# Performance work log

Hardware: AMD Instinct MI355X
Metric: run time of the kernel (lower is better)

Reference implementation:

```python
import jax, jax.numpy as jnp
import numpy as np


def _edge_index(n):
    # all ordered pairs (i, j), i != j -- static since n is a Python int
    ii = np.repeat(np.arange(n), n)
    jj = np.tile(np.arange(n), n)
    m = ii != jj
    return jnp.asarray(ii[m]), jnp.asarray(jj[m])


def _mlp2(x, w1, b1, w2, b2):
    # two Linear layers with ReLU after each (PointNet-style MLP([a,b,c]))
    h = jax.nn.relu(x @ w1 + b1)
    return jax.nn.relu(h @ w2 + b2)


def _fcn(x, w1, b1, w2, b2, w3, b3):
    # FullyConnectedNet: relu(fc1) -> relu(fc2) -> fc3 (no final relu)
    h = jax.nn.relu(x @ w1 + b1)
    h = jax.nn.relu(h @ w2 + b2)
    return h @ w3 + b3


def setup_inputs() -> dict:
    key = jax.random.key(0)
    ks = jax.random.split(key, 32)
    n = 256
    E = n * (n - 1)
    d = 512

    def lin(k, fin, fout):
        k1, k2 = jax.random.split(k)
        s = 1.0 / np.sqrt(fin)
        w = jax.random.uniform(k1, (fin, fout), jnp.float32, -s, s)
        b = jax.random.uniform(k2, (fout,), jnp.float32, -s, s)
        return w, b

    inp = {
        "insnum": n,
        "pred_codes": jax.random.normal(ks[0], (E, d), jnp.float32),
        "bboxes": jax.random.normal(ks[1], (n, 2, 3), jnp.float32),
        "lwhV": jax.random.uniform(ks[2], (n, 3), jnp.float32),
        "centroid": jax.random.normal(ks[3], (n, 3), jnp.float32),
    }
    inp["s_w1"], inp["s_b1"] = lin(ks[4], 512, 512)
    inp["s_w2"], inp["s_b2"] = lin(ks[5], 512, 512)
    inp["p_w1"], inp["p_b1"] = lin(ks[6], 512 + 128, 512)
    inp["p_w2"], inp["p_b2"] = lin(ks[7], 512, 512)
    inp["c_w1"], inp["c_b1"] = lin(ks[8], 512, 512)
    inp["c_w2"], inp["c_b2"] = lin(ks[9], 512, 512)
    inp["l_w1"], inp["l_b1"] = lin(ks[10], 512 * 3, 512)
    inp["l_w2"], inp["l_b2"] = lin(ks[11], 512, 512)
    inp["pos_w1"], inp["pos_b1"] = lin(ks[12], 5, 64)
    inp["pos_w2"], inp["pos_b2"] = lin(ks[13], 64, 64)
    inp["pos_w3"], inp["pos_b3"] = lin(ks[14], 64, 128)
    return inp


def reference(insnum, pred_codes, bboxes, lwhV, centroid,
              s_w1, s_b1, s_w2, s_b2,
              p_w1, p_b1, p_w2, p_b2,
              c_w1, c_b1, c_w2, c_b2,
              l_w1, l_b1, l_w2, l_b2,
              pos_w1, pos_b1, pos_w2, pos_b2, pos_w3, pos_b3):
    src, dst = _edge_index(insnum)
    ci = centroid[src, :2]          # [E, 2]
    cj = centroid[dst, :2]          # [E, 2]
    diff = ci - cj                  # vectorized replacement of per-edge loop
    distance = jnp.linalg.norm(diff, axis=1, keepdims=True)   # [E, 1]
    direction = diff / distance                                # [E, 2]
    pos_features = jnp.concatenate([diff, distance, direction], axis=1)  # [E, 5]

    support_codes = _mlp2(pred_codes, s_w1, s_b1, s_w2, s_b2)
    pos_codes = _fcn(pos_features, pos_w1, pos_b1, pos_w2, pos_b2, pos_w3, pos_b3)
    proximity_features = jnp.concatenate([pred_codes, pos_codes], axis=1)  # [E, 640]
    proximity_codes = _mlp2(proximity_features, p_w1, p_b1, p_w2, p_b2)
    comp_codes = _mlp2(pred_codes, c_w1, c_b1, c_w2, c_b2)
    link_in = jnp.concatenate([support_codes, proximity_codes, comp_codes], axis=1)  # [E, 1536]
    link_codes = _mlp2(link_in, l_w1, l_b1, l_w2, l_b2)
    return (link_codes, support_codes, proximity_codes, comp_codes)
```

## Files before the change

### kernel.cpp

```cpp
#include <hip/hip_runtime.h>
#include <stdint.h>

typedef unsigned short ushort_t;
typedef __attribute__((ext_vector_type(8))) short short8;
typedef __attribute__((ext_vector_type(8))) unsigned short u16x8;
typedef __attribute__((ext_vector_type(4))) float f32x4;

#define GLOBAL_AS __attribute__((address_space(1)))
#define LDS_AS __attribute__((address_space(3)))

__device__ __forceinline__ ushort_t f2bf(float f) {
  union { float f; uint32_t u; } v; v.f = f;
  uint32_t u = v.u;
  u += 0x7FFFu + ((u >> 16) & 1u);
  return (ushort_t)(u >> 16);
}

__device__ __forceinline__ int swz(int row, int byteInRow) {
  return (row * 128 + byteInRow) ^ ((row & 7) << 4);
}

struct TransArgs {
  const float* src[8];
  ushort_t* dst[8];
  int K[8];
  int blk0[9];
};

__global__ __launch_bounds__(256) void transpose_weights(TransArgs ta) {
  __shared__ float tile[64 * 65];
  int b = blockIdx.x;
  int mi = 0;
#pragma unroll
  for (int i = 1; i < 8; ++i) if (b >= ta.blk0[i]) mi = i;
  const float* src = ta.src[mi];
  ushort_t* dst = ta.dst[mi];
  int K = ta.K[mi];
  int rel = b - ta.blk0[mi];
  int ktiles = K >> 6;
  int k0 = (rel % ktiles) << 6;
  int n0 = (rel / ktiles) << 6;
  int t = threadIdx.x;
#pragma unroll
  for (int i = 0; i < 16; ++i) {
    int idx = i * 256 + t;
    int r = idx >> 6, c = idx & 63;
    tile[r * 65 + c] = src[(size_t)(k0 + r) * 512 + (n0 + c)];
  }
  __syncthreads();
#pragma unroll
  for (int i = 0; i < 16; ++i) {
    int idx = i * 256 + t;
    int r = idx >> 6, c = idx & 63;
    dst[(size_t)(n0 + r) * K + (k0 + c)] = f2bf(tile[c * 65 + r]);
  }
}

__global__ __launch_bounds__(256) void prep_kernel(
    const float* __restrict__ pred, const float* __restrict__ centroid,
    const float* __restrict__ pw1, const float* __restrict__ pb1,
    const float* __restrict__ pw2, const float* __restrict__ pb2,
    const float* __restrict__ pw3, const float* __restrict__ pb3,
    ushort_t* __restrict__ X, ushort_t* __restrict__ pos, int nm1)
{
  __shared__ ushort_t h1s[128 * 64];
  __shared__ ushort_t h2s[128 * 64];
  __shared__ ushort_t w2t[64 * 64];
  __shared__ ushort_t w3t[128 * 64];
  __shared__ float w1s[5 * 64];
  __shared__ float b1s[64], b2s[64], b3s[128];
  int t = threadIdx.x;
  for (int idx = t; idx < 64 * 64; idx += 256) {
    int k = idx >> 6, n = idx & 63;
    *(ushort_t*)((char*)w2t + swz(n, k * 2)) = f2bf(pw2[idx]);
  }
  for (int idx = t; idx < 64 * 128; idx += 256) {
    int k = idx >> 7, n = idx & 127;
    *(ushort_t*)((char*)w3t + swz(n, k * 2)) = f2bf(pw3[idx]);
  }
  for (int i = t; i < 5 * 64; i += 256) w1s[i] = pw1[i];
  if (t < 64) { b1s[t] = pb1[t]; b2s[t] = pb2[t]; }
  if (t < 128) b3s[t] = pb3[t];
  __syncthreads();

  int wid = t >> 6, lane = t & 63;
  int ebase = blockIdx.x * 128 + wid * 32;
  for (int it = 0; it < 32; ++it) {
    int e = ebase + it;
    const float* pr = pred + (size_t)e * 512 + lane * 8;
    float4 pA = *(const float4*)pr;
    float4 pB = *(const float4*)(pr + 4);
    u16x8 o;
    o[0] = f2bf(pA.x); o[1] = f2bf(pA.y); o[2] = f2bf(pA.z); o[3] = f2bf(pA.w);
    o[4] = f2bf(pB.x); o[5] = f2bf(pB.y); o[6] = f2bf(pB.z); o[7] = f2bf(pB.w);
    *(u16x8*)(X + (size_t)e * 512 + lane * 8) = o;
    int i = e / nm1;
    int r = e - i * nm1;
    int j = r + (r >= i ? 1 : 0);
    float dx = centroid[i * 3 + 0] - centroid[j * 3 + 0];
    float dy = centroid[i * 3 + 1] - centroid[j * 3 + 1];
    float dist = sqrtf(dx * dx + dy * dy);
    float inv = 1.0f / dist;
    float h1 = w1s[0 * 64 + lane] * dx + w1s[1 * 64 + lane] * dy + w1s[2 * 64 + lane] * dist
             + w1s[3 * 64 + lane] * (dx * inv) + w1s[4 * 64 + lane] * (dy * inv) + b1s[lane];
    h1 = fmaxf(h1, 0.0f);
    int row = wid * 32 + it;
    *(ushort_t*)((char*)h1s + swz(row, lane * 2)) = f2bf(h1);
  }
  __syncthreads();

  int colg = lane & 15, rowg = (lane >> 4) << 2;
  int ko_lane = (lane >> 4) * 8;
  {
    f32x4 acc[2][4];
    f32x4 zero = {0.0f, 0.0f, 0.0f, 0.0f};
#pragma unroll
    for (int m_ = 0; m_ < 2; ++m_)
#pragma unroll
      for (int n_ = 0; n_ < 4; ++n_) acc[m_][n_] = zero;
#pragma unroll
    for (int kk = 0; kk < 2; ++kk) {
      int ko = kk * 32 + ko_lane;
      short8 a[2], b[4];
#pragma unroll
      for (int m_ = 0; m_ < 2; ++m_)
        a[m_] = *(const short8*)((const char*)h1s + swz(wid * 32 + m_ * 16 + colg, ko * 2));
#pragma unroll
      for (int n_ = 0; n_ < 4; ++n_)
        b[n_] = *(const short8*)((const char*)w2t + swz(n_ * 16 + colg, ko * 2));
#pragma unroll
      for (int m_ = 0; m_ < 2; ++m_)
#pragma unroll
        for (int n_ = 0; n_ < 4; ++n_)
          acc[m_][n_] = __builtin_amdgcn_mfma_f32_16x16x32_bf16(a[m_], b[n_], acc[m_][n_], 0, 0, 0);
    }
#pragma unroll
    for (int n_ = 0; n_ < 4; ++n_) {
      int col = n_ * 16 + colg;
      float bv = b2s[col];
#pragma unroll
      for (int m_ = 0; m_ < 2; ++m_) {
        int row = wid * 32 + m_ * 16 + rowg;
#pragma unroll
        for (int jj = 0; jj < 4; ++jj) {
          float v = fmaxf(acc[m_][n_][jj] + bv, 0.0f);
          *(ushort_t*)((char*)h2s + swz(row + jj, col * 2)) = f2bf(v);
        }
      }
    }
  }
  __syncthreads();
  {
    f32x4 acc[2][8];
    f32x4 zero = {0.0f, 0.0f, 0.0f, 0.0f};
#pragma unroll
    for (int m_ = 0; m_ < 2; ++m_)
#pragma unroll
      for (int n_ = 0; n_ < 8; ++n_) acc[m_][n_] = zero;
#pragma unroll
    for (int kk = 0; kk < 2; ++kk) {
      int ko = kk * 32 + ko_lane;
      short8 a[2], b[8];
#pragma unroll
      for (int m_ = 0; m_ < 2; ++m_)
        a[m_] = *(const short8*)((const char*)h2s + swz(wid * 32 + m_ * 16 + colg, ko * 2));
#pragma unroll
      for (int n_ = 0; n_ < 8; ++n_)
        b[n_] = *(const short8*)((const char*)w3t + swz(n_ * 16 + colg, ko * 2));
#pragma unroll
      for (int m_ = 0; m_ < 2; ++m_)
#pragma unroll
        for (int n_ = 0; n_ < 8; ++n_)
          acc[m_][n_] = __builtin_amdgcn_mfma_f32_16x16x32_bf16(a[m_], b[n_], acc[m_][n_], 0, 0, 0);
    }
#pragma unroll
    for (int n_ = 0; n_ < 8; ++n_) {
      int col = n_ * 16 + colg;
      float bv = b3s[col];
#pragma unroll
      for (int m_ = 0; m_ < 2; ++m_) {
        int row = wid * 32 + m_ * 16 + rowg;
#pragma unroll
        for (int jj = 0; jj < 4; ++jj) {
          int e = blockIdx.x * 128 + row + jj;
          pos[(size_t)e * 128 + col] = f2bf(acc[m_][n_][jj] + bv);
        }
      }
    }
  }
}

__global__ __launch_bounds__(256) void gemm_bias_relu(
    const void* __restrict__ A0, int lda0,
    const void* __restrict__ A1, int lda1,
    const void* __restrict__ A2, int lda2,
    int s0, int s1, int aF32,
    const ushort_t* __restrict__ Bt, const float* __restrict__ bias,
    void* __restrict__ Cout, int outF32, ushort_t* __restrict__ Cdual, int K)
{
  __shared__ ushort_t As[128 * 64];
  __shared__ ushort_t Bs[128 * 64];
  int bid = blockIdx.x;
  int cpx = gridDim.x >> 3;
  int swzb = (bid & 7) * cpx + (bid >> 3);
  int mt = swzb >> 2, nt = swzb & 3;
  int m0 = mt << 7, n0 = nt << 7;
  int t = threadIdx.x;
  int lane = t & 63, wid = t >> 6;
  int wm = wid >> 1, wn = wid & 1;
  f32x4 acc[4][4];
  f32x4 zero = {0.0f, 0.0f, 0.0f, 0.0f};
#pragma unroll
  for (int a_ = 0; a_ < 4; ++a_)
#pragma unroll
    for (int b_ = 0; b_ < 4; ++b_) acc[a_][b_] = zero;

  for (int kt = 0; kt < K; kt += 64) {
    const void* Ab; int ldaA; int kin;
    if (kt < s0)      { Ab = A0; ldaA = lda0; kin = kt; }
    else if (kt < s1) { Ab = A1; ldaA = lda1; kin = kt - s0; }
    else              { Ab = A2; ldaA = lda2; kin = kt - s1; }
    if (aF32) {
      const float* Af = (const float*)Ab;
      int rr = t >> 1, cc0 = (t & 1) << 5;
      const float* g = Af + (size_t)(m0 + rr) * ldaA + kin + cc0;
      ushort_t* ldst = As + rr * 64 + cc0;
#pragma unroll
      for (int i = 0; i < 4; ++i) {
        float4 v0 = *(const float4*)(g + i * 8);
        float4 v1 = *(const float4*)(g + i * 8 + 4);
        u16x8 o;
        o[0] = f2bf(v0.x); o[1] = f2bf(v0.y); o[2] = f2bf(v0.z); o[3] = f2bf(v0.w);
        o[4] = f2bf(v1.x); o[5] = f2bf(v1.y); o[6] = f2bf(v1.z); o[7] = f2bf(v1.w);
        *(u16x8*)(ldst + i * 8) = o;
      }
    } else {
      const ushort_t* Ah = (const ushort_t*)Ab;
#pragma unroll
      for (int i = 0; i < 4; ++i) {
        int ch = i * 256 + t;
        int rr = ch >> 3, cc = (ch & 7) << 3;
        const ushort_t* g = Ah + (size_t)(m0 + rr) * ldaA + kin + cc;
        __builtin_amdgcn_global_load_lds((const GLOBAL_AS void*)g,
                                         (LDS_AS void*)(As + ch * 8), 16, 0, 0);
      }
    }
#pragma unroll
    for (int i = 0; i < 4; ++i) {
      int ch = i * 256 + t;
      int rr = ch >> 3, cc = (ch & 7) << 3;
      const ushort_t* g = Bt + (size_t)(n0 + rr) * K + kt + cc;
      __builtin_amdgcn_global_load_lds((const GLOBAL_AS void*)g,
                                       (LDS_AS void*)(Bs + ch * 8), 16, 0, 0);
    }
    __syncthreads();
#pragma unroll
    for (int kk = 0; kk < 64; kk += 32) {
      int ko = kk + (lane >> 4) * 8;
      short8 a[4], b[4];
#pragma unroll
      for (int m_ = 0; m_ < 4; ++m_)
        a[m_] = *(const short8*)(As + (wm * 64 + m_ * 16 + (lane & 15)) * 64 + ko);
#pragma unroll
      for (int n_ = 0; n_ < 4; ++n_)
        b[n_] = *(const short8*)(Bs + (wn * 64 + n_ * 16 + (lane & 15)) * 64 + ko);
#pragma unroll
      for (int m_ = 0; m_ < 4; ++m_)
#pragma unroll
        for (int n_ = 0; n_ < 4; ++n_)
          acc[m_][n_] = __builtin_amdgcn_mfma_f32_16x16x32_bf16(a[m_], b[n_], acc[m_][n_], 0, 0, 0);
    }
    __syncthreads();
  }
  int colg = lane & 15, rowg = (lane >> 4) << 2;
  float* C32 = (float*)Cout;
  ushort_t* C16 = (ushort_t*)Cout;
#pragma unroll
  for (int n_ = 0; n_ < 4; ++n_) {
    int col = n0 + wn * 64 + n_ * 16 + colg;
    float bv = bias[col];
#pragma unroll
    for (int m_ = 0; m_ < 4; ++m_) {
      int row = m0 + wm * 64 + m_ * 16 + rowg;
#pragma unroll
      for (int jj = 0; jj < 4; ++jj) {
        float v = fmaxf(acc[m_][n_][jj] + bv, 0.0f);
        if (outF32) C32[(size_t)(row + jj) * 512 + col] = v;
        else        C16[(size_t)(row + jj) * 512 + col] = f2bf(v);
        if (Cdual)  Cdual[(size_t)(row + jj) * 512 + col] = f2bf(v);
      }
    }
  }
}

__global__ __launch_bounds__(512, 4) void gemm128_bk32(
    const ushort_t* __restrict__ A0, int lda0,
    const ushort_t* __restrict__ A1, int lda1,
    const ushort_t* __restrict__ A2, int lda2,
    int s0, int s1,
    const ushort_t* __restrict__ Bt, const float* __restrict__ bias,
    void* __restrict__ Cout, int outF32, ushort_t* __restrict__ Cdual, int K)
{
  __shared__ char As[2 * 8192];
  __shared__ char Bs[2 * 16384];
  int bid = blockIdx.x;
  int nwg = gridDim.x;
  int q = nwg >> 3, r8_ = nwg & 7;
  int xcd = bid & 7, ii = bid >> 3;
  int sid = (xcd < r8_ ? xcd * (q + 1) : r8_ * (q + 1) + (xcd - r8_) * q) + ii;
  int mt = sid >> 1, nt = sid & 1;
  int m0 = mt << 7, n0 = nt << 8;
  int t = threadIdx.x;
  int lane = t & 63, wid = t >> 6;
  int wm = wid >> 2, wn = wid & 3;
  int g = lane >> 4, l15 = lane & 15;

  f32x4 acc[4][4];
  f32x4 zero = {0.0f, 0.0f, 0.0f, 0.0f};
#pragma unroll
  for (int mf = 0; mf < 4; ++mf)
#pragma unroll
    for (int nf = 0; nf < 4; ++nf) acc[mf][nf] = zero;

  auto stage = [&](int tile) {
    int kt = tile << 5;
    const ushort_t* src; int ld; int kin;
    if (kt < s0)      { src = A0; ld = lda0; kin = kt; }
    else if (kt < s1) { src = A1; ld = lda1; kin = kt - s0; }
    else              { src = A2; ld = lda2; kin = kt - s1; }
    char* Ad = As + (tile & 1) * 8192;
    {
      int c = t;
      int row = c >> 2;
      int sl = (c & 3) ^ (row & 3);
      const ushort_t* gp = src + (size_t)(m0 + row) * ld + kin + sl * 8;
      __builtin_amdgcn_global_load_lds((const GLOBAL_AS void*)gp,
          (LDS_AS void*)(Ad + c * 16), 16, 0, 0);
    }
    char* Bd = Bs + (tile & 1) * 16384;
#pragma unroll
    for (int L = 0; L < 2; ++L) {
      int c = wid * 128 + L * 64 + lane;
      int row = c >> 2;
      int sl = (c & 3) ^ (row & 3);
      const ushort_t* gp = Bt + (size_t)(n0 + row) * K + kt + sl * 8;
      __builtin_amdgcn_global_load_lds((const GLOBAL_AS void*)gp,
          (LDS_AS void*)(Bd + c * 16), 16, 0, 0);
    }
  };

  stage(0);
  asm volatile("s_waitcnt vmcnt(0)" ::: "memory");
  __builtin_amdgcn_s_barrier();
  __builtin_amdgcn_sched_barrier(0);

  int NT = K >> 5;
  for (int tt = 0; tt < NT; ++tt) {
    if (tt + 1 < NT) {
      stage(tt + 1);
      asm volatile("s_waitcnt vmcnt(3)" ::: "memory");
    } else {
      asm volatile("s_waitcnt vmcnt(0)" ::: "memory");
    }
    __builtin_amdgcn_s_barrier();
    __builtin_amdgcn_sched_barrier(0);
    const char* Ab = As + (tt & 1) * 8192;
    const char* Bb = Bs + (tt & 1) * 16384;
    short8 a[4], b[4];
#pragma unroll
    for (int nf = 0; nf < 4; ++nf) {
      int r = wn * 64 + nf * 16 + l15;
      b[nf] = *(const short8*)(Bb + r * 64 + ((g * 16) ^ ((r & 3) << 4)));
    }
#pragma unroll
    for (int mf = 0; mf < 4; ++mf) {
      int r = wm * 64 + mf * 16 + l15;
      a[mf] = *(const short8*)(Ab + r * 64 + ((g * 16) ^ ((r & 3) << 4)));
    }
    __builtin_amdgcn_s_setprio(1);
#pragma unroll
    for (int mf = 0; mf < 4; ++mf)
#pragma unroll
      for (int nf = 0; nf < 4; ++nf)
        acc[mf][nf] = __builtin_amdgcn_mfma_f32_16x16x32_bf16(a[mf], b[nf], acc[mf][nf], 0, 0, 0);
    __builtin_amdgcn_s_setprio(0);
    __builtin_amdgcn_sched_barrier(0);
    __builtin_amdgcn_s_barrier();
  }

  int colg = l15, rowg = g << 2;
  float* C32 = (float*)Cout;
  ushort_t* C16 = (ushort_t*)Cout;
#pragma unroll
  for (int nf = 0; nf < 4; ++nf) {
    int col = n0 + wn * 64 + nf * 16 + colg;
    float bv = bias[col];
#pragma unroll
    for (int mf = 0; mf < 4; ++mf) {
      int row = m0 + wm * 64 + mf * 16 + rowg;
#pragma unroll
      for (int jj = 0; jj < 4; ++jj) {
        float v = fmaxf(acc[mf][nf][jj] + bv, 0.0f);
        if (outF32) C32[(size_t)(row + jj) * 512 + col] = v;
        else        C16[(size_t)(row + jj) * 512 + col] = f2bf(v);
        if (Cdual)  Cdual[(size_t)(row + jj) * 512 + col] = f2bf(v);
      }
    }
  }
}

extern "C" void kernel_launch(void* const* d_in, const int* in_sizes, int n_in,
                              void* d_out, int out_size, void* d_ws, size_t ws_size,
                              hipStream_t stream) {
  (void)n_in; (void)out_size;
  const float* pred = (const float*)d_in[1];
  const float* centroid = (const float*)d_in[4];
  const float* W[8] = { (const float*)d_in[5],  (const float*)d_in[7],  (const float*)d_in[9],
                        (const float*)d_in[11], (const float*)d_in[13], (const float*)d_in[15],
                        (const float*)d_in[17], (const float*)d_in[19] };
  const float* Bv[8] = { (const float*)d_in[6],  (const float*)d_in[8],  (const float*)d_in[10],
                         (const float*)d_in[12], (const float*)d_in[14], (const float*)d_in[16],
                         (const float*)d_in[18], (const float*)d_in[20] };
  int Kd[8] = {512, 512, 640, 512, 512, 512, 1536, 512};
  const float* pos_w1 = (const float*)d_in[21]; const float* pos_b1 = (const float*)d_in[22];
  const float* pos_w2 = (const float*)d_in[23]; const float* pos_b2 = (const float*)d_in[24];
  const float* pos_w3 = (const float*)d_in[25]; const float* pos_b3 = (const float*)d_in[26];

  int E = in_sizes[1] / 512;
  int n = in_sizes[4] / 3;

  char* ws = (char*)d_ws;
  size_t off = 0;
  auto alloc = [&](size_t bytes) -> void* {
    void* p = ws + off;
    off = (off + bytes + 255) & ~(size_t)255;
    return p;
  };
  size_t SB = (size_t)E * 512 * 2;
  ushort_t* Wt[8];
  for (int i = 0; i < 8; ++i) Wt[i] = (ushort_t*)alloc((size_t)Kd[i] * 512 * 2);
  ushort_t* X = (ushort_t*)alloc(SB);
  ushort_t* Hb_ws    = (ushort_t*)alloc(SB);
  ushort_t* sup16_ws = (ushort_t*)alloc(SB);
  bool fast = (off <= ws_size) && (E % 128 == 0);

  float* outF = (float*)d_out;
  size_t S = (size_t)E * 512;
  float* out_link = outF;
  float* out_sup  = outF + S;
  float* out_prox = outF + 2 * S;
  float* out_comp = outF + 3 * S;
  ushort_t* pos = (ushort_t*)d_out;

  TransArgs ta;
  int nblk = 0;
  for (int i = 0; i < 8; ++i) {
    ta.src[i] = W[i]; ta.dst[i] = Wt[i]; ta.K[i] = Kd[i];
    ta.blk0[i] = nblk;
    nblk += (Kd[i] >> 6) * 8;
  }
  ta.blk0[8] = nblk;
  hipLaunchKernelGGL(transpose_weights, dim3(nblk), dim3(256), 0, stream, ta);
  hipLaunchKernelGGL(prep_kernel, dim3(E / 128), dim3(256), 0, stream,
                     pred, centroid, pos_w1, pos_b1, pos_w2, pos_b2, pos_w3, pos_b3,
                     X, pos, n - 1);

  const ushort_t* Zu = nullptr;
  ushort_t* NO16 = nullptr;

  if (fast) {
    dim3 g128(E / 128 * 2), b512(512);
    ushort_t* prox16 = (ushort_t*)d_out;
    ushort_t* comp16 = X;
    ushort_t* Hl = Hb_ws;
    hipLaunchKernelGGL(gemm128_bk32, g128, b512, 0, stream,
                       (const ushort_t*)X, 512, (const ushort_t*)pos, 128, Zu, 0, 512, 640,
                       Wt[2], Bv[2], (void*)Hb_ws, 0, NO16, 640);
    hipLaunchKernelGGL(gemm128_bk32, g128, b512, 0, stream,
                       (const ushort_t*)Hb_ws, 512, Zu, 0, Zu, 0, 512, 512,
                       Wt[3], Bv[3], (void*)out_prox, 1, prox16, 512);
    hipLaunchKernelGGL(gemm128_bk32, g128, b512, 0, stream,
                       (const ushort_t*)X, 512, Zu, 0, Zu, 0, 512, 512,
                       Wt[0], Bv[0], (void*)Hb_ws, 0, NO16, 512);
    hipLaunchKernelGGL(gemm128_bk32, g128, b512, 0, stream,
                       (const ushort_t*)Hb_ws, 512, Zu, 0, Zu, 0, 512, 512,
                       Wt[1], Bv[1], (void*)out_sup, 1, sup16_ws, 512);
    hipLaunchKernelGGL(gemm128_bk32, g128, b512, 0, stream,
                       (const ushort_t*)X, 512, Zu, 0, Zu, 0, 512, 512,
                       Wt[4], Bv[4], (void*)Hb_ws, 0, NO16, 512);
    hipLaunchKernelGGL(gemm128_bk32, g128, b512, 0, stream,
                       (const ushort_t*)Hb_ws, 512, Zu, 0, Zu, 0, 512, 512,
                       Wt[5], Bv[5], (void*)out_comp, 1, comp16, 512);
    hipLaunchKernelGGL(gemm128_bk32, g128, b512, 0, stream,
                       (const ushort_t*)sup16_ws, 512, (const ushort_t*)prox16, 512,
                       (const ushort_t*)comp16, 512, 512, 1024,
                       Wt[6], Bv[6], (void*)Hl, 0, NO16, 1536);
    hipLaunchKernelGGL(gemm128_bk32, g128, b512, 0, stream,
                       (const ushort_t*)Hl, 512, Zu, 0, Zu, 0, 512, 512,
                       Wt[7], Bv[7], (void*)out_link, 1, NO16, 512);
  } else {
    dim3 g(E / 128 * 4), blk(256);
    const void* Z = nullptr;
    ushort_t* Hb = (ushort_t*)((char*)d_out + (size_t)32 * 1024 * 1024);
    ushort_t* Hl = X;
    hipLaunchKernelGGL(gemm_bias_relu, g, blk, 0, stream,
                       (const void*)X, 512, (const void*)pos, 128, Z, 0, 512, 640, 0,
                       Wt[2], Bv[2], (void*)Hb, 0, NO16, 640);
    hipLaunchKernelGGL(gemm_bias_relu, g, blk, 0, stream,
                       (const void*)Hb, 512, Z, 0, Z, 0, 512, 512, 0,
                       Wt[3], Bv[3], (void*)out_prox, 1, NO16, 512);
    hipLaunchKernelGGL(gemm_bias_relu, g, blk, 0, stream,
                       (const void*)X, 512, Z, 0, Z, 0, 512, 512, 0,
                       Wt[0], Bv[0], (void*)Hb, 0, NO16, 512);
    hipLaunchKernelGGL(gemm_bias_relu, g, blk, 0, stream,
                       (const void*)Hb, 512, Z, 0, Z, 0, 512, 512, 0,
                       Wt[1], Bv[1], (void*)out_sup, 1, NO16, 512);
    hipLaunchKernelGGL(gemm_bias_relu, g, blk, 0, stream,
                       (const void*)X, 512, Z, 0, Z, 0, 512, 512, 0,
                       Wt[4], Bv[4], (void*)Hb, 0, NO16, 512);
    hipLaunchKernelGGL(gemm_bias_relu, g, blk, 0, stream,
                       (const void*)Hb, 512, Z, 0, Z, 0, 512, 512, 0,
                       Wt[5], Bv[5], (void*)out_comp, 1, NO16, 512);
    hipLaunchKernelGGL(gemm_bias_relu, g, blk, 0, stream,
                       (const void*)out_sup, 512, (const void*)out_prox, 512,
                       (const void*)out_comp, 512, 512, 1024, 1,
                       Wt[6], Bv[6], (void*)Hl, 0, NO16, 1536);
    hipLaunchKernelGGL(gemm_bias_relu, g, blk, 0, stream,
                       (const void*)Hl, 512, Z, 0, Z, 0, 512, 512, 0,
                       Wt[7], Bv[7], (void*)out_link, 1, NO16, 512);
  }
}
```

Baseline: 770.5 us.

## Keep full-K A tile resident in LDS and stream B through registers

Replaces the double-buffered K=32 GEMM with a kernel that loads the whole 128xK A slab per segment into a 128KB LDS buffer using one bulk async load. B tiles are prefetched into registers and written to a single LDS buffer each K step. The goal is to remove repeated A staging and per-tile waitcnt pipelining in favor of one-shot A residency. In exchange, the large LDS footprint cuts occupancy to one block per CU, and the extra __syncthreads per step may serialize B loads with MFMA work.

Measured after the change: 909.4 us. 1.18x slower.

```diff
diff --git a/kernel.cpp b/kernel.cpp
--- a/kernel.cpp
+++ b/kernel.cpp
@@ -293,16 +293,16 @@
   }
 }
 
-__global__ __launch_bounds__(512, 4) void gemm128_bk32(
-    const ushort_t* __restrict__ A0, int lda0,
-    const ushort_t* __restrict__ A1, int lda1,
-    const ushort_t* __restrict__ A2, int lda2,
-    int s0, int s1,
+__global__ __launch_bounds__(512) void gemm_ares(
+    const ushort_t* __restrict__ A0, int lda0, int k0,
+    const ushort_t* __restrict__ A1, int lda1, int k1,
+    const ushort_t* __restrict__ A2, int lda2, int k2,
+    int nseg,
     const ushort_t* __restrict__ Bt, const float* __restrict__ bias,
     void* __restrict__ Cout, int outF32, ushort_t* __restrict__ Cdual, int K)
 {
-  __shared__ char As[2 * 8192];
-  __shared__ char Bs[2 * 16384];
+  __shared__ char Al[131072];
+  __shared__ char Bl[16384];
   int bid = blockIdx.x;
   int nwg = gridDim.x;
   int q = nwg >> 3, r8_ = nwg & 7;
@@ -322,70 +322,75 @@
 #pragma unroll
     for (int nf = 0; nf < 4; ++nf) acc[mf][nf] = zero;
 
-  auto stage = [&](int tile) {
-    int kt = tile << 5;
-    const ushort_t* src; int ld; int kin;
-    if (kt < s0)      { src = A0; ld = lda0; kin = kt; }
-    else if (kt < s1) { src = A1; ld = lda1; kin = kt - s0; }
-    else              { src = A2; ld = lda2; kin = kt - s1; }
-    char* Ad = As + (tile & 1) * 8192;
-    {
-      int c = t;
-      int row = c >> 2;
-      int sl = (c & 3) ^ (row & 3);
-      const ushort_t* gp = src + (size_t)(m0 + row) * ld + kin + sl * 8;
-      __builtin_amdgcn_global_load_lds((const GLOBAL_AS void*)gp,
-          (LDS_AS void*)(Ad + c * 16), 16, 0, 0);
-    }
-    char* Bd = Bs + (tile & 1) * 16384;
+  auto loadB = [&](int kglob, u16x8 br[2]) {
 #pragma unroll
     for (int L = 0; L < 2; ++L) {
       int c = wid * 128 + L * 64 + lane;
-      int row = c >> 2;
-      int sl = (c & 3) ^ (row & 3);
-      const ushort_t* gp = Bt + (size_t)(n0 + row) * K + kt + sl * 8;
+      int row = c >> 2, sl = c & 3;
+      br[L] = *(const u16x8*)(Bt + (size_t)(n0 + row) * K + kglob + sl * 8);
+    }
+  };
+  auto writeB = [&](u16x8 br[2]) {
+#pragma unroll
+    for (int L = 0; L < 2; ++L) {
+      int c = wid * 128 + L * 64 + lane;
+      int row = c >> 2, sl = c & 3;
+      *(u16x8*)(Bl + row * 64 + ((sl ^ (row & 3)) << 4)) = br[L];
+    }
+  };
+
+  int kbase = 0;
+  for (int sg = 0; sg < nseg; ++sg) {
+    const ushort_t* Aseg; int lda; int Ks;
+    if (sg == 0)      { Aseg = A0; lda = lda0; Ks = k0; }
+    else if (sg == 1) { Aseg = A1; lda = lda1; Ks = k1; }
+    else              { Aseg = A2; lda = lda2; Ks = k2; }
+    int sprLog = (Ks == 512) ? 6 : 4;
+    int spr = 1 << sprLog;
+    int nload = spr >> 2;
+    for (int i = 0; i < nload; ++i) {
+      int c = i * 512 + t;
+      int row = c >> sprLog;
+      int ss = (c & (spr - 1)) ^ (row & 7);
+      const ushort_t* gp = Aseg + (size_t)(m0 + row) * lda + ss * 8;
       __builtin_amdgcn_global_load_lds((const GLOBAL_AS void*)gp,
-          (LDS_AS void*)(Bd + c * 16), 16, 0, 0);
-    }
-  };
-
-  stage(0);
-  asm volatile("s_waitcnt vmcnt(0)" ::: "memory");
-  __builtin_amdgcn_s_barrier();
-  __builtin_amdgcn_sched_barrier(0);
-
-  int NT = K >> 5;
-  for (int tt = 0; tt < NT; ++tt) {
-    if (tt + 1 < NT) {
-      stage(tt + 1);
-      asm volatile("s_waitcnt vmcnt(3)" ::: "memory");
-    } else {
-      asm volatile("s_waitcnt vmcnt(0)" ::: "memory");
-    }
-    __builtin_amdgcn_s_barrier();
-    __builtin_amdgcn_sched_barrier(0);
-    const char* Ab = As + (tt & 1) * 8192;
-    const char* Bb = Bs + (tt & 1) * 16384;
-    short8 a[4], b[4];
-#pragma unroll
-    for (int nf = 0; nf < 4; ++nf) {
-      int r = wn * 64 + nf * 16 + l15;
-      b[nf] = *(const short8*)(Bb + r * 64 + ((g * 16) ^ ((r & 3) << 4)));
-    }
-#pragma unroll
-    for (int mf = 0; mf < 4; ++mf) {
-      int r = wm * 64 + mf * 16 + l15;
-      a[mf] = *(const short8*)(Ab + r * 64 + ((g * 16) ^ ((r & 3) << 4)));
-    }
-    __builtin_amdgcn_s_setprio(1);
-#pragma unroll
-    for (int mf = 0; mf < 4; ++mf)
-#pragma unroll
-      for (int nf = 0; nf < 4; ++nf)
-        acc[mf][nf] = __builtin_amdgcn_mfma_f32_16x16x32_bf16(a[mf], b[nf], acc[mf][nf], 0, 0, 0);
-    __builtin_amdgcn_s_setprio(0);
-    __builtin_amdgcn_sched_barrier(0);
-    __builtin_amdgcn_s_barrier();
+          (LDS_AS void*)(Al + c * 16), 16, 0, 0);
+    }
+    u16x8 br[2];
+    loadB(kbase, br);
+    __syncthreads();
+    writeB(br);
+    __syncthreads();
+    int NTs = Ks >> 5;
+    int rowB = spr << 4;
+    for (int tt = 0; tt < NTs; ++tt) {
+      bool pf = (tt + 1 < NTs);
+      if (pf) loadB(kbase + (tt + 1) * 32, br);
+      short8 a[4], b[4];
+#pragma unroll
+      for (int nf = 0; nf < 4; ++nf) {
+        int r = wn * 64 + nf * 16 + l15;
+        b[nf] = *(const short8*)(Bl + r * 64 + ((g * 16) ^ ((r & 3) << 4)));
+      }
+#pragma unroll
+      for (int mf = 0; mf < 4; ++mf) {
+        int r = wm * 64 + mf * 16 + l15;
+        a[mf] = *(const short8*)(Al + r * rowB + ((tt * 64 + g * 16) ^ ((r & 7) << 4)));
+      }
+      __builtin_amdgcn_s_setprio(1);
+#pragma unroll
+      for (int mf = 0; mf < 4; ++mf)
+#pragma unroll
+        for (int nf = 0; nf < 4; ++nf)
+          acc[mf][nf] = __builtin_amdgcn_mfma_f32_16x16x32_bf16(a[mf], b[nf], acc[mf][nf], 0, 0, 0);
+      __builtin_amdgcn_s_setprio(0);
+      __syncthreads();
+      if (pf) {
+        writeB(br);
+        __syncthreads();
+      }
+    }
+    kbase += Ks;
   }
 
   int colg = l15, rowg = g << 2;
@@ -473,30 +478,31 @@
     ushort_t* prox16 = (ushort_t*)d_out;
     ushort_t* comp16 = X;
     ushort_t* Hl = Hb_ws;
-    hipLaunchKernelGGL(gemm128_bk32, g128, b512, 0, stream,
-                       (const ushort_t*)X, 512, (const ushort_t*)pos, 128, Zu, 0, 512, 640,
+    hipLaunchKernelGGL(gemm_ares, g128, b512, 0, stream,
+                       (const ushort_t*)X, 512, 512, (const ushort_t*)pos, 128, 128,
+                       Zu, 0, 0, 2,
                        Wt[2], Bv[2], (void*)Hb_ws, 0, NO16, 640);
-    hipLaunchKernelGGL(gemm128_bk32, g128, b512, 0, stream,
-                       (const ushort_t*)Hb_ws, 512, Zu, 0, Zu, 0, 512, 512,
+    hipLaunchKernelGGL(gemm_ares, g128, b512, 0, stream,
+                       (const ushort_t*)Hb_ws, 512, 512, Zu, 0, 0, Zu, 0, 0, 1,
                        Wt[3], Bv[3], (void*)out_prox, 1, prox16, 512);
-    hipLaunchKernelGGL(gemm128_bk32, g128, b512, 0, stream,
-                       (const ushort_t*)X, 512, Zu, 0, Zu, 0, 512, 512,
+    hipLaunchKernelGGL(gemm_ares, g128, b512, 0, stream,
+                       (const ushort_t*)X, 512, 512, Zu, 0, 0, Zu, 0, 0, 1,
                        Wt[0], Bv[0], (void*)Hb_ws, 0, NO16, 512);
-    hipLaunchKernelGGL(gemm128_bk32, g128, b512, 0, stream,
-                       (const ushort_t*)Hb_ws, 512, Zu, 0, Zu, 0, 512, 512,
+    hipLaunchKernelGGL(gemm_ares, g128, b512, 0, stream,
+                       (const ushort_t*)Hb_ws, 512, 512, Zu, 0, 0, Zu, 0, 0, 1,
                        Wt[1], Bv[1], (void*)out_sup, 1, sup16_ws, 512);
-    hipLaunchKernelGGL(gemm128_bk32, g128, b512, 0, stream,
-                       (const ushort_t*)X, 512, Zu, 0, Zu, 0, 512, 512,
+    hipLaunchKernelGGL(gemm_ares, g128, b512, 0, stream,
+                       (const ushort_t*)X, 512, 512, Zu, 0, 0, Zu, 0, 0, 1,
                        Wt[4], Bv[4], (void*)Hb_ws, 0, NO16, 512);
-    hipLaunchKernelGGL(gemm128_bk32, g128, b512, 0, stream,
-                       (const ushort_t*)Hb_ws, 512, Zu, 0, Zu, 0, 512, 512,
+    hipLaunchKernelGGL(gemm_ares, g128, b512, 0, stream,
+                       (const ushort_t*)Hb_ws, 512, 512, Zu, 0, 0, Zu, 0, 0, 1,
                        Wt[5], Bv[5], (void*)out_comp, 1, comp16, 512);
-    hipLaunchKernelGGL(gemm128_bk32, g128, b512, 0, stream,
-                       (const ushort_t*)sup16_ws, 512, (const ushort_t*)prox16, 512,
-                       (const ushort_t*)comp16, 512, 512, 1024,
+    hipLaunchKernelGGL(gemm_ares, g128, b512, 0, stream,
+                       (const ushort_t*)sup16_ws, 512, 512, (const ushort_t*)prox16, 512, 512,
+                       (const ushort_t*)comp16, 512, 512, 3,
                        Wt[6], Bv[6], (void*)Hl, 0, NO16, 1536);
-    hipLaunchKernelGGL(gemm128_bk32, g128, b512, 0, stream,
-                       (const ushort_t*)Hl, 512, Zu, 0, Zu, 0, 512, 512,
+    hipLaunchKernelGGL(gemm_ares, g128, b512, 0, stream,
+                       (const ushort_t*)Hl, 512, 512, Zu, 0, 0, Zu, 0, 0, 1,
                        Wt[7], Bv[7], (void*)out_link, 1, NO16, 512);
   } else {
     dim3 g(E / 128 * 4), blk(256);
```

## Batch the three independent branch MLP GEMMs into grouped multi-job launches

Applied to the files above, without the earlier changes.

Replaces eight sequential GEMM launches with four grouped launches. A job table lets a single grid run the support, proximity and comp first layers together, then their second layers together. This triples the per-launch grid and cuts the launch count, aiming to reduce tail and launch overhead. It needs extra workspace buffers (separate hidden and prox bf16 buffers), which raises memory traffic and the workspace requirement for the fast path.

After: 759.8 us. Within noise of the previous version (-1.4%).

```diff
diff --git a/kernel.cpp b/kernel.cpp
--- a/kernel.cpp
+++ b/kernel.cpp
@@ -293,20 +293,26 @@
   }
 }
 
-__global__ __launch_bounds__(512, 4) void gemm128_bk32(
-    const ushort_t* __restrict__ A0, int lda0,
-    const ushort_t* __restrict__ A1, int lda1,
-    const ushort_t* __restrict__ A2, int lda2,
-    int s0, int s1,
-    const ushort_t* __restrict__ Bt, const float* __restrict__ bias,
-    void* __restrict__ Cout, int outF32, ushort_t* __restrict__ Cdual, int K)
-{
+struct GJob {
+  const ushort_t* A0; const ushort_t* A1; const ushort_t* A2;
+  const ushort_t* Bt; const float* bias;
+  void* Cout; ushort_t* Cdual;
+  int lda0, lda1, lda2, s0, s1, K, outF32;
+};
+struct GJobs { GJob j[3]; int blk0[4]; };
+
+__global__ __launch_bounds__(512, 4) void gemm_jobs(GJobs J) {
   __shared__ char As[2 * 8192];
   __shared__ char Bs[2 * 16384];
   int bid = blockIdx.x;
-  int nwg = gridDim.x;
+  int ji = 0;
+  if (bid >= J.blk0[1]) ji = 1;
+  if (bid >= J.blk0[2]) ji = 2;
+  const GJob jb = J.j[ji];
+  int rel = bid - J.blk0[ji];
+  int nwg = J.blk0[ji + 1] - J.blk0[ji];
   int q = nwg >> 3, r8_ = nwg & 7;
-  int xcd = bid & 7, ii = bid >> 3;
+  int xcd = rel & 7, ii = rel >> 3;
   int sid = (xcd < r8_ ? xcd * (q + 1) : r8_ * (q + 1) + (xcd - r8_) * q) + ii;
   int mt = sid >> 1, nt = sid & 1;
   int m0 = mt << 7, n0 = nt << 8;
@@ -314,6 +320,7 @@
   int lane = t & 63, wid = t >> 6;
   int wm = wid >> 2, wn = wid & 3;
   int g = lane >> 4, l15 = lane & 15;
+  int K = jb.K;
 
   f32x4 acc[4][4];
   f32x4 zero = {0.0f, 0.0f, 0.0f, 0.0f};
@@ -325,9 +332,9 @@
   auto stage = [&](int tile) {
     int kt = tile << 5;
     const ushort_t* src; int ld; int kin;
-    if (kt < s0)      { src = A0; ld = lda0; kin = kt; }
-    else if (kt < s1) { src = A1; ld = lda1; kin = kt - s0; }
-    else              { src = A2; ld = lda2; kin = kt - s1; }
+    if (kt < jb.s0)      { src = jb.A0; ld = jb.lda0; kin = kt; }
+    else if (kt < jb.s1) { src = jb.A1; ld = jb.lda1; kin = kt - jb.s0; }
+    else                 { src = jb.A2; ld = jb.lda2; kin = kt - jb.s1; }
     char* Ad = As + (tile & 1) * 8192;
     {
       int c = t;
@@ -343,7 +350,7 @@
       int c = wid * 128 + L * 64 + lane;
       int row = c >> 2;
       int sl = (c & 3) ^ (row & 3);
-      const ushort_t* gp = Bt + (size_t)(n0 + row) * K + kt + sl * 8;
+      const ushort_t* gp = jb.Bt + (size_t)(n0 + row) * K + kt + sl * 8;
       __builtin_amdgcn_global_load_lds((const GLOBAL_AS void*)gp,
           (LDS_AS void*)(Bd + c * 16), 16, 0, 0);
     }
@@ -389,21 +396,22 @@
   }
 
   int colg = l15, rowg = g << 2;
-  float* C32 = (float*)Cout;
-  ushort_t* C16 = (ushort_t*)Cout;
+  float* C32 = (float*)jb.Cout;
+  ushort_t* C16 = (ushort_t*)jb.Cout;
+  ushort_t* Cdual = jb.Cdual;
 #pragma unroll
   for (int nf = 0; nf < 4; ++nf) {
     int col = n0 + wn * 64 + nf * 16 + colg;
-    float bv = bias[col];
+    float bv = jb.bias[col];
 #pragma unroll
     for (int mf = 0; mf < 4; ++mf) {
       int row = m0 + wm * 64 + mf * 16 + rowg;
 #pragma unroll
       for (int jj = 0; jj < 4; ++jj) {
         float v = fmaxf(acc[mf][nf][jj] + bv, 0.0f);
-        if (outF32) C32[(size_t)(row + jj) * 512 + col] = v;
-        else        C16[(size_t)(row + jj) * 512 + col] = f2bf(v);
-        if (Cdual)  Cdual[(size_t)(row + jj) * 512 + col] = f2bf(v);
+        if (jb.outF32) C32[(size_t)(row + jj) * 512 + col] = v;
+        else           C16[(size_t)(row + jj) * 512 + col] = f2bf(v);
+        if (Cdual)     Cdual[(size_t)(row + jj) * 512 + col] = f2bf(v);
       }
     }
   }
@@ -440,8 +448,11 @@
   ushort_t* Wt[8];
   for (int i = 0; i < 8; ++i) Wt[i] = (ushort_t*)alloc((size_t)Kd[i] * 512 * 2);
   ushort_t* X = (ushort_t*)alloc(SB);
-  ushort_t* Hb_ws    = (ushort_t*)alloc(SB);
-  ushort_t* sup16_ws = (ushort_t*)alloc(SB);
+  ushort_t* Hb_sup  = (ushort_t*)alloc(SB);
+  ushort_t* Hb_prox = (ushort_t*)alloc(SB);
+  ushort_t* Hb_comp = (ushort_t*)alloc(SB);
+  ushort_t* sup16_ws  = (ushort_t*)alloc(SB);
+  ushort_t* prox16_ws = (ushort_t*)alloc(SB);
   bool fast = (off <= ws_size) && (E % 128 == 0);
 
   float* outF = (float*)d_out;
@@ -469,35 +480,49 @@
   ushort_t* NO16 = nullptr;
 
   if (fast) {
-    dim3 g128(E / 128 * 2), b512(512);
-    ushort_t* prox16 = (ushort_t*)d_out;
+    int nb = E / 128 * 2;
+    dim3 b512(512);
     ushort_t* comp16 = X;
-    ushort_t* Hl = Hb_ws;
-    hipLaunchKernelGGL(gemm128_bk32, g128, b512, 0, stream,
-                       (const ushort_t*)X, 512, (const ushort_t*)pos, 128, Zu, 0, 512, 640,
-                       Wt[2], Bv[2], (void*)Hb_ws, 0, NO16, 640);
-    hipLaunchKernelGGL(gemm128_bk32, g128, b512, 0, stream,
-                       (const ushort_t*)Hb_ws, 512, Zu, 0, Zu, 0, 512, 512,
-                       Wt[3], Bv[3], (void*)out_prox, 1, prox16, 512);
-    hipLaunchKernelGGL(gemm128_bk32, g128, b512, 0, stream,
-                       (const ushort_t*)X, 512, Zu, 0, Zu, 0, 512, 512,
-                       Wt[0], Bv[0], (void*)Hb_ws, 0, NO16, 512);
-    hipLaunchKernelGGL(gemm128_bk32, g128, b512, 0, stream,
-                       (const ushort_t*)Hb_ws, 512, Zu, 0, Zu, 0, 512, 512,
-                       Wt[1], Bv[1], (void*)out_sup, 1, sup16_ws, 512);
-    hipLaunchKernelGGL(gemm128_bk32, g128, b512, 0, stream,
-                       (const ushort_t*)X, 512, Zu, 0, Zu, 0, 512, 512,
-                       Wt[4], Bv[4], (void*)Hb_ws, 0, NO16, 512);
-    hipLaunchKernelGGL(gemm128_bk32, g128, b512, 0, stream,
-                       (const ushort_t*)Hb_ws, 512, Zu, 0, Zu, 0, 512, 512,
-                       Wt[5], Bv[5], (void*)out_comp, 1, comp16, 512);
-    hipLaunchKernelGGL(gemm128_bk32, g128, b512, 0, stream,
-                       (const ushort_t*)sup16_ws, 512, (const ushort_t*)prox16, 512,
-                       (const ushort_t*)comp16, 512, 512, 1024,
-                       Wt[6], Bv[6], (void*)Hl, 0, NO16, 1536);
-    hipLaunchKernelGGL(gemm128_bk32, g128, b512, 0, stream,
-                       (const ushort_t*)Hl, 512, Zu, 0, Zu, 0, 512, 512,
-                       Wt[7], Bv[7], (void*)out_link, 1, NO16, 512);
+    ushort_t* Hl = Hb_sup;
+
+    auto mkjob = [&](const ushort_t* A0, int lda0, const ushort_t* A1, int lda1,
+                     const ushort_t* A2, int lda2, int s0, int s1,
+                     const ushort_t* Bt, const float* bias,
+                     void* Cout, ushort_t* dual, int K, int outF32) {
+      GJob j;
+      j.A0 = A0; j.A1 = A1; j.A2 = A2; j.Bt = Bt; j.bias = bias;
+      j.Cout = Cout; j.Cdual = dual;
+      j.lda0 = lda0; j.lda1 = lda1; j.lda2 = lda2;
+      j.s0 = s0; j.s1 = s1; j.K = K; j.outF32 = outF32;
+      return j;
+    };
+
+    GJobs JA;
+    JA.j[0] = mkjob(X, 512, Zu, 0, Zu, 0, 512, 512, Wt[0], Bv[0], Hb_sup,  NO16, 512, 0);
+    JA.j[1] = mkjob(X, 512, pos, 128, Zu, 0, 512, 640, Wt[2], Bv[2], Hb_prox, NO16, 640, 0);
+    JA.j[2] = mkjob(X, 512, Zu, 0, Zu, 0, 512, 512, Wt[4], Bv[4], Hb_comp, NO16, 512, 0);
+    JA.blk0[0] = 0; JA.blk0[1] = nb; JA.blk0[2] = 2 * nb; JA.blk0[3] = 3 * nb;
+    hipLaunchKernelGGL(gemm_jobs, dim3(3 * nb), b512, 0, stream, JA);
+
+    GJobs JB;
+    JB.j[0] = mkjob(Hb_sup,  512, Zu, 0, Zu, 0, 512, 512, Wt[1], Bv[1], out_sup,  sup16_ws,  512, 1);
+    JB.j[1] = mkjob(Hb_prox, 512, Zu, 0, Zu, 0, 512, 512, Wt[3], Bv[3], out_prox, prox16_ws, 512, 1);
+    JB.j[2] = mkjob(Hb_comp, 512, Zu, 0, Zu, 0, 512, 512, Wt[5], Bv[5], out_comp, comp16,    512, 1);
+    JB.blk0[0] = 0; JB.blk0[1] = nb; JB.blk0[2] = 2 * nb; JB.blk0[3] = 3 * nb;
+    hipLaunchKernelGGL(gemm_jobs, dim3(3 * nb), b512, 0, stream, JB);
+
+    GJobs JC;
+    JC.j[0] = mkjob(sup16_ws, 512, prox16_ws, 512, comp16, 512, 512, 1024,
+                    Wt[6], Bv[6], Hl, NO16, 1536, 0);
+    JC.j[1] = JC.j[0]; JC.j[2] = JC.j[0];
+    JC.blk0[0] = 0; JC.blk0[1] = nb; JC.blk0[2] = nb; JC.blk0[3] = nb;
+    hipLaunchKernelGGL(gemm_jobs, dim3(nb), b512, 0, stream, JC);
+
+    GJobs JD;
+    JD.j[0] = mkjob(Hl, 512, Zu, 0, Zu, 0, 512, 512, Wt[7], Bv[7], out_link, NO16, 512, 1);
+    JD.j[1] = JD.j[0]; JD.j[2] = JD.j[0];
+    JD.blk0[0] = 0; JD.blk0[1] = nb; JD.blk0[2] = nb; JD.blk0[3] = nb;
+    hipLaunchKernelGGL(gemm_jobs, dim3(nb), b512, 0, stream, JD);
   } else {
     dim3 g(E / 128 * 4), blk(256);
     const void* Z = nullptr;
```
